# Kernel tuning notes

Measured on AMD Instinct MI355X. Metric: run time of the kernel, lower is better.

The kernel has to match this reference:

```python
import jax, jax.numpy as jnp
import numpy as np

N, E = 50000, 800000
IN_DIM, OUT_DIM, H = 256, 128, 8
GEO_HID = 16  # RBF feature dim and geo_mlp hidden dim


def setup_inputs() -> dict:
    key = jax.random.key(0)
    ks = jax.random.split(key, 16)
    def lin(k, fan_out, fan_in):
        kw, kb = jax.random.split(k)
        lim = 1.0 / np.sqrt(fan_in)
        W = jax.random.uniform(kw, (fan_out, fan_in), jnp.float32, -lim, lim)
        b = jax.random.uniform(kb, (fan_out,), jnp.float32, -lim, lim)
        return W, b
    Wq, bq = lin(ks[0], OUT_DIM, IN_DIM)
    Wk, bk = lin(ks[1], OUT_DIM, IN_DIM)
    Wv, bv = lin(ks[2], OUT_DIM, IN_DIM)
    Wo, bo = lin(ks[3], OUT_DIM, OUT_DIM)
    Wg1, bg1 = lin(ks[4], GEO_HID, GEO_HID)
    Wg2, bg2 = lin(ks[5], H, GEO_HID)
    x = jax.random.normal(ks[6], (N, IN_DIM), jnp.float32)
    edge_index = jax.random.randint(ks[7], (2, E), 0, N, jnp.int64)
    edge_dist = jax.random.uniform(ks[8], (E,), jnp.float32) * 6.0
    return {"x": x, "edge_index": edge_index, "edge_dist": edge_dist,
            "Wq": Wq, "bq": bq, "Wk": Wk, "bk": bk, "Wv": Wv, "bv": bv,
            "Wo": Wo, "bo": bo, "Wg1": Wg1, "bg1": bg1, "Wg2": Wg2, "bg2": bg2}


def reference(x, edge_index, edge_dist, Wq, bq, Wk, bk, Wv, bv, Wo, bo, Wg1, bg1, Wg2, bg2):
    n = x.shape[0]
    num_heads = Wg2.shape[0]
    head_dim = Wq.shape[0] // num_heads
    scale = 1.0 / (head_dim ** 0.5)

    q = (x @ Wq.T + bq).reshape(n, num_heads, head_dim)
    k = (x @ Wk.T + bk).reshape(n, num_heads, head_dim)
    v = (x @ Wv.T + bv).reshape(n, num_heads, head_dim)

    # RBF expansion: 16 centers in [0, 6], gamma = 1.0
    centers = jnp.linspace(0.0, 6.0, GEO_HID)
    rbf = jnp.exp(-(edge_dist[:, None] - centers) ** 2)          # [E, 16]
    geo_bias = jax.nn.relu(rbf @ Wg1.T + bg1) @ Wg2.T + bg2      # [E, H]

    row, col = edge_index[0], edge_index[1]
    attn = (q[row] * k[col]).sum(-1) * scale + geo_bias          # [E, H]

    # segment softmax over incoming edges per destination node (row)
    m = jax.ops.segment_max(attn, row, num_segments=n)           # [N, H]
    e = jnp.exp(attn - m[row])
    s = jax.ops.segment_sum(e, row, num_segments=n)              # [N, H]
    a = e / (s[row] + 1e-12)                                     # [E, H]

    out = jax.ops.segment_sum(v[col] * a[:, :, None], row, num_segments=n)
    out = out.reshape(n, num_heads * head_dim)
    return out @ Wo.T + bo
```

## Files before the change

kernel.cpp:

```cpp
#include <hip/hip_runtime.h>
#include <math.h>

#define IN_DIM 256
#define OUT_DIM 128
#define NH 8
#define HD 16
#define GH 16
#define TBL 1024
#define LOG2E 1.44269504f
#define RCAP 64
#define BCAP 2560

typedef __attribute__((ext_vector_type(8))) short short8;
typedef __attribute__((ext_vector_type(4))) float floatx4;

__device__ __forceinline__ unsigned short f2bf(float f) {
    union { float f; unsigned u; } v; v.f = f;
    unsigned r = v.u + 0x7fffu + ((v.u >> 16) & 1u);
    return (unsigned short)(r >> 16);
}
__device__ __forceinline__ float bf2f(unsigned short h) {
    union { unsigned u; float f; } v; v.u = ((unsigned)h) << 16;
    return v.f;
}
__device__ __forceinline__ void split1(float f, unsigned short& h, unsigned short& l) {
    h = f2bf(f);
    l = f2bf(f - bf2f(h));
}
__device__ __forceinline__ float bflo(unsigned u) { return __uint_as_float(u << 16); }
__device__ __forceinline__ float bfhi(unsigned u) { return __uint_as_float(u & 0xffff0000u); }

__global__ __launch_bounds__(256) void prep_all_kernel(
    const float* __restrict__ x, const float* __restrict__ Wq, const float* __restrict__ Wk,
    const float* __restrict__ Wv, const float* __restrict__ Wo,
    unsigned short* __restrict__ xh, unsigned short* __restrict__ xl,
    unsigned short* __restrict__ wh, unsigned short* __restrict__ wl,
    unsigned short* __restrict__ wo_h, unsigned short* __restrict__ wo_l,
    const float* __restrict__ Wg1, const float* __restrict__ bg1,
    const float* __restrict__ Wg2, const float* __restrict__ bg2,
    float* __restrict__ tbl, int* __restrict__ gbin,
    int n4x, int nbins, int nsplit, int nwm, int nwo, int ngeo) {
    int bx = blockIdx.x;
    int t = threadIdx.x;

    if (bx < nsplit) {
        int i = bx * 256 + t;
        if (i >= n4x) return;
        float4 f = ((const float4*)x)[i];
        ushort4 h, l;
        split1(f.x, h.x, l.x); split1(f.y, h.y, l.y);
        split1(f.z, h.z, l.z); split1(f.w, h.w, l.w);
        ((ushort4*)xh)[i] = h;
        ((ushort4*)xl)[i] = l;
        return;
    }
    bx -= nsplit;
    if (bx < 3 * nwm) {
        int m = bx / nwm;
        int i = (bx - m * nwm) * 256 + t;
        if (i >= (OUT_DIM * IN_DIM) / 4) return;
        const float* W = (m == 0) ? Wq : (m == 1) ? Wk : Wv;
        float4 f = ((const float4*)W)[i];
        ushort4 h, l;
        split1(f.x, h.x, l.x); split1(f.y, h.y, l.y);
        split1(f.z, h.z, l.z); split1(f.w, h.w, l.w);
        size_t base = (size_t)m * (OUT_DIM * IN_DIM) / 4;
        ((ushort4*)wh)[base + i] = h;
        ((ushort4*)wl)[base + i] = l;
        return;
    }
    bx -= 3 * nwm;
    if (bx < nwo) {
        int i = bx * 256 + t;
        if (i >= (OUT_DIM * OUT_DIM) / 4) return;
        float4 f = ((const float4*)Wo)[i];
        ushort4 h, l;
        split1(f.x, h.x, l.x); split1(f.y, h.y, l.y);
        split1(f.z, h.z, l.z); split1(f.w, h.w, l.w);
        ((ushort4*)wo_h)[i] = h;
        ((ushort4*)wo_l)[i] = l;
        return;
    }
    bx -= nwo;
    if (bx < ngeo) {
        int i = bx * 256 + t;
        if (i >= TBL) return;
        float d = (float)i * (6.0f / (float)(TBL - 1));
        float rbf[GH];
#pragma unroll
        for (int j = 0; j < GH; ++j) {
            float c = 0.4f * (float)j;
            float tt = d - c;
            rbf[j] = __expf(-tt * tt);
        }
        float hid[GH];
#pragma unroll
        for (int j = 0; j < GH; ++j) {
            float acc = bg1[j];
#pragma unroll
            for (int kk = 0; kk < GH; ++kk) acc += rbf[kk] * Wg1[j * GH + kk];
            hid[j] = fmaxf(acc, 0.0f);
        }
#pragma unroll
        for (int h = 0; h < NH; ++h) {
            float acc = bg2[h];
#pragma unroll
            for (int j = 0; j < GH; ++j) acc += hid[j] * Wg2[h * GH + j];
            tbl[i * NH + h] = acc * LOG2E;
        }
        return;
    }
    for (int i = t; i < nbins; i += 256) gbin[i] = 0;
}

__global__ __launch_bounds__(512, 4) void qkv_kernel(
    const unsigned short* __restrict__ xh, const unsigned short* __restrict__ xl,
    const unsigned short* __restrict__ wh, const unsigned short* __restrict__ wl,
    const float* __restrict__ bq, const float* __restrict__ bk, const float* __restrict__ bv,
    float* __restrict__ q, unsigned short* __restrict__ kb, unsigned short* __restrict__ vb,
    const int* __restrict__ ei, const float* __restrict__ edist,
    int* __restrict__ gbin, int2* __restrict__ binbuf,
    int Nn, int E_, int nxb, int nb1, int nbins) {
    __shared__ unsigned short xh_s[128 * 40];
    __shared__ unsigned short xl_s[128 * 40];
    __shared__ unsigned short wh_s[128 * 40];
    __shared__ unsigned short wl_s[128 * 40];

    const int tid = threadIdx.x;
    int bx = blockIdx.x;

    if (bx < nb1) {
        int* hist = (int*)xh_s;
        const int e0 = bx * 4096;
        for (int b = tid; b < nbins; b += 512) hist[b] = 0;
        __syncthreads();
#pragma unroll
        for (int i = 0; i < 8; ++i) {
            int e = e0 + tid + i * 512;
            if (e < E_) atomicAdd(&hist[ei[e] >> 7], 1);
        }
        __syncthreads();
        for (int b = tid; b < nbins; b += 512) {
            int h = hist[b];
            int base = 0;
            if (h) base = atomicAdd(&gbin[b], h);
            hist[b] = base;
        }
        __syncthreads();
#pragma unroll
        for (int i = 0; i < 8; ++i) {
            int e = e0 + tid + i * 512;
            if (e < E_) {
                int row = ei[e];
                int bin = row >> 7;
                int r = atomicAdd(&hist[bin], 1);
                float u = edist[e] * ((float)(TBL - 1) / 6.0f);
                u = fminf(fmaxf(u, 0.0f), (float)(TBL - 1));
                if (r < BCAP)
                    binbuf[(size_t)bin * BCAP + r] =
                        make_int2((ei[E_ + e] & 0x1FFFF) | ((row & 127) << 17), __float_as_int(u));
            }
        }
        return;
    }
    bx -= nb1;

    const int wsel = bx / nxb;
    const int n0 = (bx - wsel * nxb) * 128;
    const unsigned short* W_h = wh + (size_t)wsel * (OUT_DIM * IN_DIM);
    const unsigned short* W_l = wl + (size_t)wsel * (OUT_DIM * IN_DIM);
    const float* bias = (wsel == 0) ? bq : (wsel == 1) ? bk : bv;
    const bool vpath = (wsel == 2);

    const int w = tid >> 6;
    const int lane = tid & 63;
    const int ml = lane & 15;
    const int quad = lane >> 4;
    const int rg = w & 3;
    const int cg = w >> 2;

    const int rows_valid = min(128, Nn - n0);

    floatx4 acc[2][4];
#pragma unroll
    for (int rr = 0; rr < 2; ++rr)
#pragma unroll
        for (int ct = 0; ct < 4; ++ct) acc[rr][ct] = (floatx4){0.f, 0.f, 0.f, 0.f};

    const short8 zero8 = {0, 0, 0, 0, 0, 0, 0, 0};

    for (int kc = 0; kc < IN_DIM; kc += 32) {
        {
            int r = tid >> 2, c = tid & 3;
            size_t gx = (size_t)(n0 + r) * IN_DIM + kc + c * 8;
            size_t gw = (size_t)r * IN_DIM + kc + c * 8;
            short8 vh = zero8;
            if (r < rows_valid) vh = *(const short8*)(xh + gx);
            *(short8*)(xh_s + r * 40 + c * 8) = vh;
            *(short8*)(wh_s + r * 40 + c * 8) = *(const short8*)(W_h + gw);
            if (vpath) {
                short8 vl = zero8;
                if (r < rows_valid) vl = *(const short8*)(xl + gx);
                *(short8*)(xl_s + r * 40 + c * 8) = vl;
                *(short8*)(wl_s + r * 40 + c * 8) = *(const short8*)(W_l + gw);
            }
        }
        __syncthreads();

        short8 ah0 = *(const short8*)(xh_s + (rg * 32 + ml) * 40 + quad * 8);
        short8 ah1 = *(const short8*)(xh_s + (rg * 32 + 16 + ml) * 40 + quad * 8);
        if (!vpath) {
#pragma unroll
            for (int ct = 0; ct < 4; ++ct) {
                short8 bh = *(const short8*)(wh_s + (cg * 64 + ct * 16 + ml) * 40 + quad * 8);
                acc[0][ct] = __builtin_amdgcn_mfma_f32_16x16x32_bf16(ah0, bh, acc[0][ct], 0, 0, 0);
                acc[1][ct] = __builtin_amdgcn_mfma_f32_16x16x32_bf16(ah1, bh, acc[1][ct], 0, 0, 0);
            }
        } else {
            short8 al0 = *(const short8*)(xl_s + (rg * 32 + ml) * 40 + quad * 8);
            short8 al1 = *(const short8*)(xl_s + (rg * 32 + 16 + ml) * 40 + quad * 8);
#pragma unroll
            for (int ct = 0; ct < 4; ++ct) {
                short8 bh = *(const short8*)(wh_s + (cg * 64 + ct * 16 + ml) * 40 + quad * 8);
                short8 bl = *(const short8*)(wl_s + (cg * 64 + ct * 16 + ml) * 40 + quad * 8);
                acc[0][ct] = __builtin_amdgcn_mfma_f32_16x16x32_bf16(ah0, bh, acc[0][ct], 0, 0, 0);
                acc[0][ct] = __builtin_amdgcn_mfma_f32_16x16x32_bf16(al0, bh, acc[0][ct], 0, 0, 0);
                acc[0][ct] = __builtin_amdgcn_mfma_f32_16x16x32_bf16(ah0, bl, acc[0][ct], 0, 0, 0);
                acc[1][ct] = __builtin_amdgcn_mfma_f32_16x16x32_bf16(ah1, bh, acc[1][ct], 0, 0, 0);
                acc[1][ct] = __builtin_amdgcn_mfma_f32_16x16x32_bf16(al1, bh, acc[1][ct], 0, 0, 0);
                acc[1][ct] = __builtin_amdgcn_mfma_f32_16x16x32_bf16(ah1, bl, acc[1][ct], 0, 0, 0);
            }
        }
        __syncthreads();
    }

    if (wsel == 0) {
#pragma unroll
        for (int rr = 0; rr < 2; ++rr)
#pragma unroll
            for (int ct = 0; ct < 4; ++ct) {
                int col = cg * 64 + ct * 16 + ml;
                float bj = bias[col];
#pragma unroll
                for (int r = 0; r < 4; ++r) {
                    int grow = n0 + rg * 32 + rr * 16 + quad * 4 + r;
                    if (grow < Nn) q[(size_t)grow * 128 + col] = acc[rr][ct][r] + bj;
                }
            }
    } else {
        unsigned short* ob = (wsel == 1) ? kb : vb;
#pragma unroll
        for (int rr = 0; rr < 2; ++rr)
#pragma unroll
            for (int ct = 0; ct < 4; ++ct) {
                int col = cg * 64 + ct * 16 + ml;
                float bj = bias[col];
#pragma unroll
                for (int r = 0; r < 4; ++r) {
                    int grow = n0 + rg * 32 + rr * 16 + quad * 4 + r;
                    if (grow < Nn) ob[(size_t)grow * 128 + col] = f2bf(acc[rr][ct][r] + bj);
                }
            }
    }
}

__global__ __launch_bounds__(256) void bin2bucket_kernel(
    const int2* __restrict__ binbuf, const int* __restrict__ gbin,
    int2* __restrict__ bucket, int2* __restrict__ meta, int Nn) {
    __shared__ int rcnt[128];
    __shared__ int pref[128];
    __shared__ int2 ebuf[BCAP];
    const int bin = blockIdx.x;
    const int t = threadIdx.x;
    if (t < 128) rcnt[t] = 0;
    __syncthreads();
    int nb = gbin[bin];
    if (nb > BCAP) nb = BCAP;
    const int row0 = bin << 7;

    int px[10], py[10], rk[10];
#pragma unroll
    for (int j = 0; j < 10; ++j) {
        int i = t + j * 256;
        rk[j] = -1;
        if (i < nb) {
            int2 p = binbuf[(size_t)bin * BCAP + i];
            int rowrel = (p.x >> 17) & 127;
            int r = atomicAdd(&rcnt[rowrel], 1);
            if (r < RCAP) { px[j] = p.x & 0x1FFFF; py[j] = p.y; rk[j] = r | (rowrel << 16); }
        }
    }
    __syncthreads();
    int myclamp = 0;
    if (t < 128) { myclamp = min(rcnt[t], RCAP); pref[t] = myclamp; }
    __syncthreads();
    for (int off = 1; off < 128; off <<= 1) {
        int v = 0;
        if (t < 128 && t >= off) v = pref[t - off];
        __syncthreads();
        if (t < 128) pref[t] += v;
        __syncthreads();
    }
#pragma unroll
    for (int j = 0; j < 10; ++j) {
        if (rk[j] >= 0) {
            int rowrel = rk[j] >> 16;
            int r = rk[j] & 0xFFFF;
            int pos = pref[rowrel] - min(rcnt[rowrel], RCAP) + r;
            ebuf[pos] = make_int2(px[j], py[j]);
        }
    }
    __syncthreads();
    int total = pref[127];
    const int obase = bin * BCAP;
    for (int i = t; i < total; i += 256) bucket[obase + i] = ebuf[i];
    if (t < 128 && row0 + t < Nn)
        meta[row0 + t] = make_int2(obase + pref[t] - myclamp, myclamp);
}

__global__ __launch_bounds__(256) void fused_node_kernel(
    const float* __restrict__ q, const unsigned short* __restrict__ kb,
    const unsigned short* __restrict__ vb, const int2* __restrict__ bucket,
    const float* __restrict__ tbl, const int2* __restrict__ meta,
    float* __restrict__ o, int Nn, int nwav) {
    const int lane = threadIdx.x & 63;
    const int g = lane >> 3;
    const int h = lane & 7;
    int wid = blockIdx.x * (blockDim.x >> 6) + (threadIdx.x >> 6);
    if (wid >= Nn) return;

    int2 mnext = meta[wid];
    for (int n = wid; n < Nn; n += nwav) {
        const int2 m = mnext;
        const int n2 = n + nwav;
        if (n2 < Nn) mnext = meta[n2];

        const int start = m.x;
        const int c = m.y;
        const int end = start + c;

        float qf[16];
        {
            const float4* qp = (const float4*)(q + (size_t)n * 128 + h * 16);
#pragma unroll
            for (int j = 0; j < 4; ++j) {
                float4 t = qp[j];
                qf[j * 4 + 0] = t.x; qf[j * 4 + 1] = t.y;
                qf[j * 4 + 2] = t.z; qf[j * 4 + 3] = t.w;
            }
        }

        float l = 0.0f;
        float acc[16];
#pragma unroll
        for (int j = 0; j < 16; ++j) acc[j] = 0.0f;

        auto edge_math = [&](const uint4& k0, const uint4& k1, const uint4& v0, const uint4& v1,
                             float u, bool valid) {
            unsigned kk[8] = {k0.x, k0.y, k0.z, k0.w, k1.x, k1.y, k1.z, k1.w};
            float d = 0.0f;
#pragma unroll
            for (int j = 0; j < 8; ++j) {
                d = fmaf(bflo(kk[j]), qf[2 * j], d);
                d = fmaf(bfhi(kk[j]), qf[2 * j + 1], d);
            }
            int i0 = min((int)u, TBL - 2);
            float fr = u - (float)i0;
            float t0 = tbl[i0 * NH + h];
            float t1 = tbl[i0 * NH + NH + h];
            float logit2 = fmaf(d, 0.25f * LOG2E, fmaf(fr, t1 - t0, t0));
            logit2 = fminf(logit2, 80.0f);
            if (!valid) logit2 = -1e30f;
            float p = __builtin_amdgcn_exp2f(logit2);
            l += p;
            unsigned vv[8] = {v0.x, v0.y, v0.z, v0.w, v1.x, v1.y, v1.z, v1.w};
#pragma unroll
            for (int j = 0; j < 8; ++j) {
                acc[2 * j]     = fmaf(p, bflo(vv[j]), acc[2 * j]);
                acc[2 * j + 1] = fmaf(p, bfhi(vv[j]), acc[2 * j + 1]);
            }
        };

        if (c > 0) {
            int2 npA = bucket[min(start + g, end - 1)];
            const bool vAv = (start + g < end);
            const bool doB = (end > start + 8);
            int2 npB = npA;
            bool vBv = false;
            if (doB) {
                npB = bucket[min(start + 8 + g, end - 1)];
                vBv = (start + 8 + g < end);
            }
            const uint4* kpA = (const uint4*)(kb + (size_t)npA.x * 128 + h * 16);
            const uint4* vpA = (const uint4*)(vb + (size_t)npA.x * 128 + h * 16);
            uint4 kA0 = kpA[0], kA1 = kpA[1], vA0 = vpA[0], vA1 = vpA[1];
            uint4 kB0, kB1, vB0, vB1;
            if (doB) {
                const uint4* kpB = (const uint4*)(kb + (size_t)npB.x * 128 + h * 16);
                const uint4* vpB = (const uint4*)(vb + (size_t)npB.x * 128 + h * 16);
                kB0 = kpB[0]; kB1 = kpB[1]; vB0 = vpB[0]; vB1 = vpB[1];
            }
            edge_math(kA0, kA1, vA0, vA1, __int_as_float(npA.y), vAv);
            if (doB) edge_math(kB0, kB1, vB0, vB1, __int_as_float(npB.y), vBv);
            for (int base = start + 16; base < end; base += 8) {
                int2 np = bucket[min(base + g, end - 1)];
                bool valid = (base + g < end);
                const uint4* kp = (const uint4*)(kb + (size_t)np.x * 128 + h * 16);
                const uint4* vp = (const uint4*)(vb + (size_t)np.x * 128 + h * 16);
                uint4 k0 = kp[0], k1 = kp[1], v0 = vp[0], v1 = vp[1];
                edge_math(k0, k1, v0, v1, __int_as_float(np.y), valid);
            }
        }

#pragma unroll
        for (int off = 8; off < 64; off <<= 1) {
            l += __shfl_xor(l, off);
#pragma unroll
            for (int j = 0; j < 16; ++j) acc[j] += __shfl_xor(acc[j], off);
        }

        if (g == 0) {
            float inv = 1.0f / (l + 1e-12f);
            float4* op = (float4*)(o + (size_t)n * 128 + h * 16);
#pragma unroll
            for (int j = 0; j < 4; ++j) {
                float4 t;
                t.x = acc[j * 4 + 0] * inv; t.y = acc[j * 4 + 1] * inv;
                t.z = acc[j * 4 + 2] * inv; t.w = acc[j * 4 + 3] * inv;
                op[j] = t;
            }
        }
    }
}

__global__ __launch_bounds__(512, 4) void out_gemm_mfma_kernel(
    const float* __restrict__ o,
    const unsigned short* __restrict__ wo_h, const unsigned short* __restrict__ wo_l,
    const float* __restrict__ bo, float* __restrict__ out, int Nn) {
    const int n0 = blockIdx.x * 128;

    __shared__ unsigned short xh_s[128 * 40];
    __shared__ unsigned short xl_s[128 * 40];
    __shared__ unsigned short wh_s[128 * 40];
    __shared__ unsigned short wl_s[128 * 40];

    const int tid = threadIdx.x;
    const int w = tid >> 6;
    const int lane = tid & 63;
    const int ml = lane & 15;
    const int quad = lane >> 4;
    const int rg = w & 3;
    const int cg = w >> 2;

    const int rows_valid = min(128, Nn - n0);

    floatx4 acc[2][4];
#pragma unroll
    for (int rr = 0; rr < 2; ++rr)
#pragma unroll
        for (int ct = 0; ct < 4; ++ct) acc[rr][ct] = (floatx4){0.f, 0.f, 0.f, 0.f};

    for (int kc = 0; kc < OUT_DIM; kc += 32) {
        {
            int r = tid >> 2, c = tid & 3;
            unsigned short hv[8], lv[8];
            if (r < rows_valid) {
                const float* src = o + (size_t)(n0 + r) * OUT_DIM + kc + c * 8;
#pragma unroll
                for (int j = 0; j < 8; ++j) split1(src[j], hv[j], lv[j]);
            } else {
#pragma unroll
                for (int j = 0; j < 8; ++j) { hv[j] = 0; lv[j] = 0; }
            }
            *(short8*)(xh_s + r * 40 + c * 8) = *(short8*)hv;
            *(short8*)(xl_s + r * 40 + c * 8) = *(short8*)lv;
            size_t gg = (size_t)r * OUT_DIM + kc + c * 8;
            *(short8*)(wh_s + r * 40 + c * 8) = *(const short8*)(wo_h + gg);
            *(short8*)(wl_s + r * 40 + c * 8) = *(const short8*)(wo_l + gg);
        }
        __syncthreads();

        short8 ah0 = *(const short8*)(xh_s + (rg * 32 + ml) * 40 + quad * 8);
        short8 ah1 = *(const short8*)(xh_s + (rg * 32 + 16 + ml) * 40 + quad * 8);
        short8 al0 = *(const short8*)(xl_s + (rg * 32 + ml) * 40 + quad * 8);
        short8 al1 = *(const short8*)(xl_s + (rg * 32 + 16 + ml) * 40 + quad * 8);
#pragma unroll
        for (int ct = 0; ct < 4; ++ct) {
            short8 bh = *(const short8*)(wh_s + (cg * 64 + ct * 16 + ml) * 40 + quad * 8);
            short8 bl = *(const short8*)(wl_s + (cg * 64 + ct * 16 + ml) * 40 + quad * 8);
            acc[0][ct] = __builtin_amdgcn_mfma_f32_16x16x32_bf16(ah0, bh, acc[0][ct], 0, 0, 0);
            acc[0][ct] = __builtin_amdgcn_mfma_f32_16x16x32_bf16(al0, bh, acc[0][ct], 0, 0, 0);
            acc[0][ct] = __builtin_amdgcn_mfma_f32_16x16x32_bf16(ah0, bl, acc[0][ct], 0, 0, 0);
            acc[1][ct] = __builtin_amdgcn_mfma_f32_16x16x32_bf16(ah1, bh, acc[1][ct], 0, 0, 0);
            acc[1][ct] = __builtin_amdgcn_mfma_f32_16x16x32_bf16(al1, bh, acc[1][ct], 0, 0, 0);
            acc[1][ct] = __builtin_amdgcn_mfma_f32_16x16x32_bf16(ah1, bl, acc[1][ct], 0, 0, 0);
        }
        __syncthreads();
    }

#pragma unroll
    for (int rr = 0; rr < 2; ++rr)
#pragma unroll
        for (int ct = 0; ct < 4; ++ct) {
            int col = cg * 64 + ct * 16 + ml;
            float bj = bo[col];
#pragma unroll
            for (int r = 0; r < 4; ++r) {
                int grow = n0 + rg * 32 + rr * 16 + quad * 4 + r;
                if (grow < Nn) out[(size_t)grow * 128 + col] = acc[rr][ct][r] + bj;
            }
        }
}

extern "C" void kernel_launch(void* const* d_in, const int* in_sizes, int n_in,
                              void* d_out, int out_size, void* d_ws, size_t ws_size,
                              hipStream_t stream) {
    const float* x   = (const float*)d_in[0];
    const int* ei    = (const int*)d_in[1];
    const float* edist = (const float*)d_in[2];
    const float* Wq = (const float*)d_in[3];  const float* bq = (const float*)d_in[4];
    const float* Wk = (const float*)d_in[5];  const float* bk = (const float*)d_in[6];
    const float* Wv = (const float*)d_in[7];  const float* bv = (const float*)d_in[8];
    const float* Wo = (const float*)d_in[9];  const float* bo = (const float*)d_in[10];
    const float* Wg1 = (const float*)d_in[11]; const float* bg1 = (const float*)d_in[12];
    const float* Wg2 = (const float*)d_in[13]; const float* bg2 = (const float*)d_in[14];
    const int Nn = in_sizes[0] / IN_DIM;
    const int Ee = in_sizes[2];
    float* out = (float*)d_out;

    char* ws = (char*)d_ws;
    size_t off = 0;
    auto alloc = [&](size_t bytes) -> char* {
        char* p = ws + off;
        off += (bytes + 255) & ~(size_t)255;
        return p;
    };
    float* q  = (float*)alloc((size_t)Nn * 128 * 4);
    unsigned short* kbuf = (unsigned short*)alloc((size_t)Nn * 128 * 2);
    unsigned short* vbuf = (unsigned short*)alloc((size_t)Nn * 128 * 2);
    char* xlblock = alloc((size_t)Nn * IN_DIM * 2);
    float* o = (float*)alloc((size_t)Nn * 128 * 4);
    float* geot = (float*)alloc((size_t)TBL * 8 * 4);
    int2* meta = (int2*)alloc((size_t)Nn * 8);
    int nbins = (Nn + 127) >> 7;
    int* gbin = (int*)alloc((size_t)nbins * 4);
    unsigned short* wh_all = (unsigned short*)alloc((size_t)3 * OUT_DIM * IN_DIM * 2);
    unsigned short* wl_all = (unsigned short*)alloc((size_t)3 * OUT_DIM * IN_DIM * 2);
    unsigned short* wo_h = (unsigned short*)alloc((size_t)OUT_DIM * OUT_DIM * 2);
    unsigned short* wo_l = (unsigned short*)alloc((size_t)OUT_DIM * OUT_DIM * 2);
    int2* bucket = (int2*)alloc((size_t)nbins * BCAP * 8);

    int2* binbuf = (int2*)o;

    unsigned short* xh = (unsigned short*)d_out;
    unsigned short* xl = (unsigned short*)xlblock;

    int n4x = Nn * IN_DIM / 4;
    int nsplit = (n4x + 255) / 256;
    int nwm = ((OUT_DIM * IN_DIM / 4) + 255) / 256;
    int nwo = ((OUT_DIM * OUT_DIM / 4) + 255) / 256;
    int ngeo = (TBL + 255) / 256;
    int gprep = nsplit + 3 * nwm + nwo + ngeo + 1;
    prep_all_kernel<<<gprep, 256, 0, stream>>>(
        x, Wq, Wk, Wv, Wo, xh, xl, wh_all, wl_all, wo_h, wo_l,
        Wg1, bg1, Wg2, bg2, geot, gbin, n4x, nbins, nsplit, nwm, nwo, ngeo);

    int nxb = (Nn + 127) / 128;
    int nb1 = (Ee + 4095) / 4096;
    qkv_kernel<<<nb1 + 3 * nxb, 512, 0, stream>>>(
        xh, xl, wh_all, wl_all, bq, bk, bv, q, kbuf, vbuf,
        ei, edist, gbin, binbuf, Nn, Ee, nxb, nb1, nbins);

    bin2bucket_kernel<<<nbins, 256, 0, stream>>>(binbuf, gbin, bucket, meta, Nn);

    {
        int nblk = 2048;
        int nwav = nblk * 4;
        fused_node_kernel<<<nblk, 256, 0, stream>>>(q, kbuf, vbuf, bucket, geot, meta, o, Nn, nwav);
    }

    out_gemm_mfma_kernel<<<(Nn + 127) / 128, 512, 0, stream>>>(o, wo_h, wo_l, bo, out, Nn);
}
```

Measured before the change: 267.7 us.

## Fuse x bf16 split into QKV GEMM, halve bin size, one node per wave

Drops the separate pass that split x into bf16 hi/lo arrays. The QKV GEMM now loads fp32 x directly and converts it in registers, which removes a full write and reread of the split x buffers. Edge bins shrink from 128 to 64 rows with a smaller capacity, doubling the number of bucket blocks and cutting per-block shared memory and register arrays. The attention kernel switches from a grid-stride persistent loop to one node per wave, which adds more blocks but removes the prefetch logic. The cost is that every row tile of the x conversion is repeated across the three QKV weight blocks.

New measurement: 254.4 us. 5.0% less time.

```diff
diff --git a/kernel.cpp b/kernel.cpp
--- a/kernel.cpp
+++ b/kernel.cpp
@@ -9,7 +9,8 @@
 #define TBL 1024
 #define LOG2E 1.44269504f
 #define RCAP 64
-#define BCAP 2560
+#define BINSH 6
+#define BCAP 1408
 
 typedef __attribute__((ext_vector_type(8))) short short8;
 typedef __attribute__((ext_vector_type(4))) float floatx4;
@@ -31,30 +32,17 @@
 __device__ __forceinline__ float bfhi(unsigned u) { return __uint_as_float(u & 0xffff0000u); }
 
 __global__ __launch_bounds__(256) void prep_all_kernel(
-    const float* __restrict__ x, const float* __restrict__ Wq, const float* __restrict__ Wk,
+    const float* __restrict__ Wq, const float* __restrict__ Wk,
     const float* __restrict__ Wv, const float* __restrict__ Wo,
-    unsigned short* __restrict__ xh, unsigned short* __restrict__ xl,
     unsigned short* __restrict__ wh, unsigned short* __restrict__ wl,
     unsigned short* __restrict__ wo_h, unsigned short* __restrict__ wo_l,
     const float* __restrict__ Wg1, const float* __restrict__ bg1,
     const float* __restrict__ Wg2, const float* __restrict__ bg2,
     float* __restrict__ tbl, int* __restrict__ gbin,
-    int n4x, int nbins, int nsplit, int nwm, int nwo, int ngeo) {
+    int nbins, int nwm, int nwo, int ngeo) {
     int bx = blockIdx.x;
     int t = threadIdx.x;
 
-    if (bx < nsplit) {
-        int i = bx * 256 + t;
-        if (i >= n4x) return;
-        float4 f = ((const float4*)x)[i];
-        ushort4 h, l;
-        split1(f.x, h.x, l.x); split1(f.y, h.y, l.y);
-        split1(f.z, h.z, l.z); split1(f.w, h.w, l.w);
-        ((ushort4*)xh)[i] = h;
-        ((ushort4*)xl)[i] = l;
-        return;
-    }
-    bx -= nsplit;
     if (bx < 3 * nwm) {
         int m = bx / nwm;
         int i = (bx - m * nwm) * 256 + t;
@@ -114,7 +102,7 @@
 }
 
 __global__ __launch_bounds__(512, 4) void qkv_kernel(
-    const unsigned short* __restrict__ xh, const unsigned short* __restrict__ xl,
+    const float* __restrict__ x,
     const unsigned short* __restrict__ wh, const unsigned short* __restrict__ wl,
     const float* __restrict__ bq, const float* __restrict__ bk, const float* __restrict__ bv,
     float* __restrict__ q, unsigned short* __restrict__ kb, unsigned short* __restrict__ vb,
@@ -137,7 +125,7 @@
 #pragma unroll
         for (int i = 0; i < 8; ++i) {
             int e = e0 + tid + i * 512;
-            if (e < E_) atomicAdd(&hist[ei[e] >> 7], 1);
+            if (e < E_) atomicAdd(&hist[ei[e] >> BINSH], 1);
         }
         __syncthreads();
         for (int b = tid; b < nbins; b += 512) {
@@ -152,13 +140,13 @@
             int e = e0 + tid + i * 512;
             if (e < E_) {
                 int row = ei[e];
-                int bin = row >> 7;
+                int bin = row >> BINSH;
                 int r = atomicAdd(&hist[bin], 1);
                 float u = edist[e] * ((float)(TBL - 1) / 6.0f);
                 u = fminf(fmaxf(u, 0.0f), (float)(TBL - 1));
                 if (r < BCAP)
                     binbuf[(size_t)bin * BCAP + r] =
-                        make_int2((ei[E_ + e] & 0x1FFFF) | ((row & 127) << 17), __float_as_int(u));
+                        make_int2((ei[E_ + e] & 0x1FFFF) | ((row & 63) << 17), __float_as_int(u));
             }
         }
         return;
@@ -187,21 +175,33 @@
 #pragma unroll
         for (int ct = 0; ct < 4; ++ct) acc[rr][ct] = (floatx4){0.f, 0.f, 0.f, 0.f};
 
-    const short8 zero8 = {0, 0, 0, 0, 0, 0, 0, 0};
-
     for (int kc = 0; kc < IN_DIM; kc += 32) {
         {
             int r = tid >> 2, c = tid & 3;
-            size_t gx = (size_t)(n0 + r) * IN_DIM + kc + c * 8;
+            float xf[8];
+            if (r < rows_valid) {
+                const float4* xs = (const float4*)(x + (size_t)(n0 + r) * IN_DIM + kc + c * 8);
+                float4 a = xs[0], b = xs[1];
+                xf[0] = a.x; xf[1] = a.y; xf[2] = a.z; xf[3] = a.w;
+                xf[4] = b.x; xf[5] = b.y; xf[6] = b.z; xf[7] = b.w;
+            } else {
+#pragma unroll
+                for (int j = 0; j < 8; ++j) xf[j] = 0.0f;
+            }
             size_t gw = (size_t)r * IN_DIM + kc + c * 8;
-            short8 vh = zero8;
-            if (r < rows_valid) vh = *(const short8*)(xh + gx);
-            *(short8*)(xh_s + r * 40 + c * 8) = vh;
-            *(short8*)(wh_s + r * 40 + c * 8) = *(const short8*)(W_h + gw);
-            if (vpath) {
-                short8 vl = zero8;
-                if (r < rows_valid) vl = *(const short8*)(xl + gx);
-                *(short8*)(xl_s + r * 40 + c * 8) = vl;
+            if (!vpath) {
+                unsigned short hv[8];
+#pragma unroll
+                for (int j = 0; j < 8; ++j) hv[j] = f2bf(xf[j]);
+                *(short8*)(xh_s + r * 40 + c * 8) = *(short8*)hv;
+                *(short8*)(wh_s + r * 40 + c * 8) = *(const short8*)(W_h + gw);
+            } else {
+                unsigned short hv[8], lv[8];
+#pragma unroll
+                for (int j = 0; j < 8; ++j) split1(xf[j], hv[j], lv[j]);
+                *(short8*)(xh_s + r * 40 + c * 8) = *(short8*)hv;
+                *(short8*)(xl_s + r * 40 + c * 8) = *(short8*)lv;
+                *(short8*)(wh_s + r * 40 + c * 8) = *(const short8*)(W_h + gw);
                 *(short8*)(wl_s + r * 40 + c * 8) = *(const short8*)(W_l + gw);
             }
         }
@@ -267,42 +267,42 @@
 __global__ __launch_bounds__(256) void bin2bucket_kernel(
     const int2* __restrict__ binbuf, const int* __restrict__ gbin,
     int2* __restrict__ bucket, int2* __restrict__ meta, int Nn) {
-    __shared__ int rcnt[128];
-    __shared__ int pref[128];
+    __shared__ int rcnt[64];
+    __shared__ int pref[64];
     __shared__ int2 ebuf[BCAP];
     const int bin = blockIdx.x;
     const int t = threadIdx.x;
-    if (t < 128) rcnt[t] = 0;
+    if (t < 64) rcnt[t] = 0;
     __syncthreads();
     int nb = gbin[bin];
     if (nb > BCAP) nb = BCAP;
-    const int row0 = bin << 7;
-
-    int px[10], py[10], rk[10];
-#pragma unroll
-    for (int j = 0; j < 10; ++j) {
+    const int row0 = bin << BINSH;
+
+    int px[6], py[6], rk[6];
+#pragma unroll
+    for (int j = 0; j < 6; ++j) {
         int i = t + j * 256;
         rk[j] = -1;
         if (i < nb) {
             int2 p = binbuf[(size_t)bin * BCAP + i];
-            int rowrel = (p.x >> 17) & 127;
+            int rowrel = (p.x >> 17) & 63;
             int r = atomicAdd(&rcnt[rowrel], 1);
             if (r < RCAP) { px[j] = p.x & 0x1FFFF; py[j] = p.y; rk[j] = r | (rowrel << 16); }
         }
     }
     __syncthreads();
     int myclamp = 0;
-    if (t < 128) { myclamp = min(rcnt[t], RCAP); pref[t] = myclamp; }
+    if (t < 64) { myclamp = min(rcnt[t], RCAP); pref[t] = myclamp; }
     __syncthreads();
-    for (int off = 1; off < 128; off <<= 1) {
+    for (int off = 1; off < 64; off <<= 1) {
         int v = 0;
-        if (t < 128 && t >= off) v = pref[t - off];
-        __syncthreads();
-        if (t < 128) pref[t] += v;
-        __syncthreads();
-    }
-#pragma unroll
-    for (int j = 0; j < 10; ++j) {
+        if (t < 64 && t >= off) v = pref[t - off];
+        __syncthreads();
+        if (t < 64) pref[t] += v;
+        __syncthreads();
+    }
+#pragma unroll
+    for (int j = 0; j < 6; ++j) {
         if (rk[j] >= 0) {
             int rowrel = rk[j] >> 16;
             int r = rk[j] & 0xFFFF;
@@ -311,10 +311,10 @@
         }
     }
     __syncthreads();
-    int total = pref[127];
+    int total = pref[63];
     const int obase = bin * BCAP;
     for (int i = t; i < total; i += 256) bucket[obase + i] = ebuf[i];
-    if (t < 128 && row0 + t < Nn)
+    if (t < 64 && row0 + t < Nn)
         meta[row0 + t] = make_int2(obase + pref[t] - myclamp, myclamp);
 }
 
@@ -322,113 +322,107 @@
     const float* __restrict__ q, const unsigned short* __restrict__ kb,
     const unsigned short* __restrict__ vb, const int2* __restrict__ bucket,
     const float* __restrict__ tbl, const int2* __restrict__ meta,
-    float* __restrict__ o, int Nn, int nwav) {
+    float* __restrict__ o, int Nn) {
     const int lane = threadIdx.x & 63;
     const int g = lane >> 3;
     const int h = lane & 7;
-    int wid = blockIdx.x * (blockDim.x >> 6) + (threadIdx.x >> 6);
-    if (wid >= Nn) return;
-
-    int2 mnext = meta[wid];
-    for (int n = wid; n < Nn; n += nwav) {
-        const int2 m = mnext;
-        const int n2 = n + nwav;
-        if (n2 < Nn) mnext = meta[n2];
-
-        const int start = m.x;
-        const int c = m.y;
-        const int end = start + c;
-
-        float qf[16];
-        {
-            const float4* qp = (const float4*)(q + (size_t)n * 128 + h * 16);
-#pragma unroll
-            for (int j = 0; j < 4; ++j) {
-                float4 t = qp[j];
-                qf[j * 4 + 0] = t.x; qf[j * 4 + 1] = t.y;
-                qf[j * 4 + 2] = t.z; qf[j * 4 + 3] = t.w;
-            }
-        }
-
-        float l = 0.0f;
-        float acc[16];
-#pragma unroll
-        for (int j = 0; j < 16; ++j) acc[j] = 0.0f;
-
-        auto edge_math = [&](const uint4& k0, const uint4& k1, const uint4& v0, const uint4& v1,
-                             float u, bool valid) {
-            unsigned kk[8] = {k0.x, k0.y, k0.z, k0.w, k1.x, k1.y, k1.z, k1.w};
-            float d = 0.0f;
-#pragma unroll
-            for (int j = 0; j < 8; ++j) {
-                d = fmaf(bflo(kk[j]), qf[2 * j], d);
-                d = fmaf(bfhi(kk[j]), qf[2 * j + 1], d);
-            }
-            int i0 = min((int)u, TBL - 2);
-            float fr = u - (float)i0;
-            float t0 = tbl[i0 * NH + h];
-            float t1 = tbl[i0 * NH + NH + h];
-            float logit2 = fmaf(d, 0.25f * LOG2E, fmaf(fr, t1 - t0, t0));
-            logit2 = fminf(logit2, 80.0f);
-            if (!valid) logit2 = -1e30f;
-            float p = __builtin_amdgcn_exp2f(logit2);
-            l += p;
-            unsigned vv[8] = {v0.x, v0.y, v0.z, v0.w, v1.x, v1.y, v1.z, v1.w};
-#pragma unroll
-            for (int j = 0; j < 8; ++j) {
-                acc[2 * j]     = fmaf(p, bflo(vv[j]), acc[2 * j]);
-                acc[2 * j + 1] = fmaf(p, bfhi(vv[j]), acc[2 * j + 1]);
-            }
-        };
-
-        if (c > 0) {
-            int2 npA = bucket[min(start + g, end - 1)];
-            const bool vAv = (start + g < end);
-            const bool doB = (end > start + 8);
-            int2 npB = npA;
-            bool vBv = false;
-            if (doB) {
-                npB = bucket[min(start + 8 + g, end - 1)];
-                vBv = (start + 8 + g < end);
-            }
-            const uint4* kpA = (const uint4*)(kb + (size_t)npA.x * 128 + h * 16);
-            const uint4* vpA = (const uint4*)(vb + (size_t)npA.x * 128 + h * 16);
-            uint4 kA0 = kpA[0], kA1 = kpA[1], vA0 = vpA[0], vA1 = vpA[1];
-            uint4 kB0, kB1, vB0, vB1;
-            if (doB) {
-                const uint4* kpB = (const uint4*)(kb + (size_t)npB.x * 128 + h * 16);
-                const uint4* vpB = (const uint4*)(vb + (size_t)npB.x * 128 + h * 16);
-                kB0 = kpB[0]; kB1 = kpB[1]; vB0 = vpB[0]; vB1 = vpB[1];
-            }
-            edge_math(kA0, kA1, vA0, vA1, __int_as_float(npA.y), vAv);
-            if (doB) edge_math(kB0, kB1, vB0, vB1, __int_as_float(npB.y), vBv);
-            for (int base = start + 16; base < end; base += 8) {
-                int2 np = bucket[min(base + g, end - 1)];
-                bool valid = (base + g < end);
-                const uint4* kp = (const uint4*)(kb + (size_t)np.x * 128 + h * 16);
-                const uint4* vp = (const uint4*)(vb + (size_t)np.x * 128 + h * 16);
-                uint4 k0 = kp[0], k1 = kp[1], v0 = vp[0], v1 = vp[1];
-                edge_math(k0, k1, v0, v1, __int_as_float(np.y), valid);
-            }
-        }
-
-#pragma unroll
-        for (int off = 8; off < 64; off <<= 1) {
-            l += __shfl_xor(l, off);
-#pragma unroll
-            for (int j = 0; j < 16; ++j) acc[j] += __shfl_xor(acc[j], off);
-        }
-
-        if (g == 0) {
-            float inv = 1.0f / (l + 1e-12f);
-            float4* op = (float4*)(o + (size_t)n * 128 + h * 16);
-#pragma unroll
-            for (int j = 0; j < 4; ++j) {
-                float4 t;
-                t.x = acc[j * 4 + 0] * inv; t.y = acc[j * 4 + 1] * inv;
-                t.z = acc[j * 4 + 2] * inv; t.w = acc[j * 4 + 3] * inv;
-                op[j] = t;
-            }
+    const int n = blockIdx.x * 4 + (threadIdx.x >> 6);
+    if (n >= Nn) return;
+
+    const int2 m = meta[n];
+    const int start = m.x;
+    const int c = m.y;
+    const int end = start + c;
+
+    float qf[16];
+    {
+        const float4* qp = (const float4*)(q + (size_t)n * 128 + h * 16);
+#pragma unroll
+        for (int j = 0; j < 4; ++j) {
+            float4 t = qp[j];
+            qf[j * 4 + 0] = t.x; qf[j * 4 + 1] = t.y;
+            qf[j * 4 + 2] = t.z; qf[j * 4 + 3] = t.w;
+        }
+    }
+
+    float l = 0.0f;
+    float acc[16];
+#pragma unroll
+    for (int j = 0; j < 16; ++j) acc[j] = 0.0f;
+
+    auto edge_math = [&](const uint4& k0, const uint4& k1, const uint4& v0, const uint4& v1,
+                         float u, bool valid) {
+        unsigned kk[8] = {k0.x, k0.y, k0.z, k0.w, k1.x, k1.y, k1.z, k1.w};
+        float d = 0.0f;
+#pragma unroll
+        for (int j = 0; j < 8; ++j) {
+            d = fmaf(bflo(kk[j]), qf[2 * j], d);
+            d = fmaf(bfhi(kk[j]), qf[2 * j + 1], d);
+        }
+        int i0 = min((int)u, TBL - 2);
+        float fr = u - (float)i0;
+        float t0 = tbl[i0 * NH + h];
+        float t1 = tbl[i0 * NH + NH + h];
+        float logit2 = fmaf(d, 0.25f * LOG2E, fmaf(fr, t1 - t0, t0));
+        logit2 = fminf(logit2, 80.0f);
+        if (!valid) logit2 = -1e30f;
+        float p = __builtin_amdgcn_exp2f(logit2);
+        l += p;
+        unsigned vv[8] = {v0.x, v0.y, v0.z, v0.w, v1.x, v1.y, v1.z, v1.w};
+#pragma unroll
+        for (int j = 0; j < 8; ++j) {
+            acc[2 * j]     = fmaf(p, bflo(vv[j]), acc[2 * j]);
+            acc[2 * j + 1] = fmaf(p, bfhi(vv[j]), acc[2 * j + 1]);
+        }
+    };
+
+    if (c > 0) {
+        int2 npA = bucket[min(start + g, end - 1)];
+        const bool vAv = (start + g < end);
+        const bool doB = (end > start + 8);
+        int2 npB = npA;
+        bool vBv = false;
+        if (doB) {
+            npB = bucket[min(start + 8 + g, end - 1)];
+            vBv = (start + 8 + g < end);
+        }
+        const uint4* kpA = (const uint4*)(kb + (size_t)npA.x * 128 + h * 16);
+        const uint4* vpA = (const uint4*)(vb + (size_t)npA.x * 128 + h * 16);
+        uint4 kA0 = kpA[0], kA1 = kpA[1], vA0 = vpA[0], vA1 = vpA[1];
+        uint4 kB0, kB1, vB0, vB1;
+        if (doB) {
+            const uint4* kpB = (const uint4*)(kb + (size_t)npB.x * 128 + h * 16);
+            const uint4* vpB = (const uint4*)(vb + (size_t)npB.x * 128 + h * 16);
+            kB0 = kpB[0]; kB1 = kpB[1]; vB0 = vpB[0]; vB1 = vpB[1];
+        }
+        edge_math(kA0, kA1, vA0, vA1, __int_as_float(npA.y), vAv);
+        if (doB) edge_math(kB0, kB1, vB0, vB1, __int_as_float(npB.y), vBv);
+        for (int base = start + 16; base < end; base += 8) {
+            int2 np = bucket[min(base + g, end - 1)];
+            bool valid = (base + g < end);
+            const uint4* kp = (const uint4*)(kb + (size_t)np.x * 128 + h * 16);
+            const uint4* vp = (const uint4*)(vb + (size_t)np.x * 128 + h * 16);
+            uint4 k0 = kp[0], k1 = kp[1], v0 = vp[0], v1 = vp[1];
+            edge_math(k0, k1, v0, v1, __int_as_float(np.y), valid);
+        }
+    }
+
+#pragma unroll
+    for (int off = 8; off < 64; off <<= 1) {
+        l += __shfl_xor(l, off);
+#pragma unroll
+        for (int j = 0; j < 16; ++j) acc[j] += __shfl_xor(acc[j], off);
+    }
+
+    if (g == 0) {
+        float inv = 1.0f / (l + 1e-12f);
+        float4* op = (float4*)(o + (size_t)n * 128 + h * 16);
+#pragma unroll
+        for (int j = 0; j < 4; ++j) {
+            float4 t;
+            t.x = acc[j * 4 + 0] * inv; t.y = acc[j * 4 + 1] * inv;
+            t.z = acc[j * 4 + 2] * inv; t.w = acc[j * 4 + 3] * inv;
+            op[j] = t;
         }
     }
 }
@@ -538,11 +532,10 @@
     float* q  = (float*)alloc((size_t)Nn * 128 * 4);
     unsigned short* kbuf = (unsigned short*)alloc((size_t)Nn * 128 * 2);
     unsigned short* vbuf = (unsigned short*)alloc((size_t)Nn * 128 * 2);
-    char* xlblock = alloc((size_t)Nn * IN_DIM * 2);
     float* o = (float*)alloc((size_t)Nn * 128 * 4);
     float* geot = (float*)alloc((size_t)TBL * 8 * 4);
     int2* meta = (int2*)alloc((size_t)Nn * 8);
-    int nbins = (Nn + 127) >> 7;
+    int nbins = (Nn + 63) >> BINSH;
     int* gbin = (int*)alloc((size_t)nbins * 4);
     unsigned short* wh_all = (unsigned short*)alloc((size_t)3 * OUT_DIM * IN_DIM * 2);
     unsigned short* wl_all = (unsigned short*)alloc((size_t)3 * OUT_DIM * IN_DIM * 2);
@@ -552,32 +545,23 @@
 
     int2* binbuf = (int2*)o;
 
-    unsigned short* xh = (unsigned short*)d_out;
-    unsigned short* xl = (unsigned short*)xlblock;
-
-    int n4x = Nn * IN_DIM / 4;
-    int nsplit = (n4x + 255) / 256;
     int nwm = ((OUT_DIM * IN_DIM / 4) + 255) / 256;
     int nwo = ((OUT_DIM * OUT_DIM / 4) + 255) / 256;
     int ngeo = (TBL + 255) / 256;
-    int gprep = nsplit + 3 * nwm + nwo + ngeo + 1;
+    int gprep = 3 * nwm + nwo + ngeo + 1;
     prep_all_kernel<<<gprep, 256, 0, stream>>>(
-        x, Wq, Wk, Wv, Wo, xh, xl, wh_all, wl_all, wo_h, wo_l,
-        Wg1, bg1, Wg2, bg2, geot, gbin, n4x, nbins, nsplit, nwm, nwo, ngeo);
+        Wq, Wk, Wv, Wo, wh_all, wl_all, wo_h, wo_l,
+        Wg1, bg1, Wg2, bg2, geot, gbin, nbins, nwm, nwo, ngeo);
 
     int nxb = (Nn + 127) / 128;
     int nb1 = (Ee + 4095) / 4096;
     qkv_kernel<<<nb1 + 3 * nxb, 512, 0, stream>>>(
-        xh, xl, wh_all, wl_all, bq, bk, bv, q, kbuf, vbuf,
+        x, wh_all, wl_all, bq, bk, bv, q, kbuf, vbuf,
         ei, edist, gbin, binbuf, Nn, Ee, nxb, nb1, nbins);
 
     bin2bucket_kernel<<<nbins, 256, 0, stream>>>(binbuf, gbin, bucket, meta, Nn);
 
-    {
-        int nblk = 2048;
-        int nwav = nblk * 4;
-        fused_node_kernel<<<nblk, 256, 0, stream>>>(q, kbuf, vbuf, bucket, geot, meta, o, Nn, nwav);
-    }
+    fused_node_kernel<<<(Nn + 3) / 4, 256, 0, stream>>>(q, kbuf, vbuf, bucket, geot, meta, o, Nn);
 
     out_gemm_mfma_kernel<<<(Nn + 127) / 128, 512, 0, stream>>>(o, wo_h, wo_l, bo, out, Nn);
 }
```
